# Performance work log

Hardware: AMD Instinct MI355X
Metric: run time of the kernel (lower is better)

Reference implementation:

```python
import jax, jax.numpy as jnp
import numpy as np

D_MODEL = 128
NHEAD = 8
NLAYERS = 6
LAYER_NAMES = ['self', 'cross', 'self', 'cross', 'self', 'cross']
TEMPERATURE = 5.0
EPS = 1e-6


def _pos_encoding(x):
    # Sinusoidal 1D position encoding along the width axis. x: [N, H, W, C]
    C, W = x.shape[-1], x.shape[2]
    pos = jnp.arange(W, dtype=x.dtype)[:, None]                      # [W,1]
    div = jnp.exp(jnp.arange(0, C, 2, dtype=x.dtype) * (-np.log(10000.0) / C))
    pe = jnp.zeros((W, C), x.dtype)
    pe = pe.at[:, 0::2].set(jnp.sin(pos * div))
    pe = pe.at[:, 1::2].set(jnp.cos(pos * div))
    return x + pe[None, None]                                        # broadcast over N,H


def _linear_attention(q, k, v):
    # q,k,v: [N, H, W, nhead, dim]; kernelized linear attention along W
    Q = jax.nn.elu(q) + 1.0
    K = jax.nn.elu(k) + 1.0
    v_len = v.shape[2]
    V = v / v_len
    KV = jnp.einsum('nhsed,nhsev->nhedv', K, V)                      # [N,H,e,d,d]
    Z = 1.0 / (jnp.einsum('nhled,nhed->nhle', Q, K.sum(axis=2)) + EPS)
    return jnp.einsum('nhled,nhedv,nhle->nhlev', Q, KV, Z) * v_len


def _layer_norm(x, g, b):
    m = x.mean(-1, keepdims=True)
    v = jnp.mean((x - m) ** 2, -1, keepdims=True)
    return (x - m) / jnp.sqrt(v + 1e-5) * g + b


def _encoder_layer(x, source, Wq, Wk, Wv, Wm, W1, W2, g1, b1, g2, b2):
    x = _pos_encoding(x)
    source = _pos_encoding(source)
    bs, h, w, c = x.shape
    e, d = NHEAD, c // NHEAD
    q = (x @ Wq).reshape(bs, h, w, e, d)
    k = (source @ Wk).reshape(bs, h, w, e, d)
    v = (source @ Wv).reshape(bs, h, w, e, d)
    msg = _linear_attention(q, k, v).reshape(bs, h, w, c) @ Wm
    msg = _layer_norm(msg, g1, b1)
    msg = jnp.concatenate([x, msg], axis=-1)                         # [N,H,W,2C]
    msg = jax.nn.relu(msg @ W1) @ W2
    msg = _layer_norm(msg, g2, b2)
    return x + msg


def _forward(feat0, feat1, Wq, Wk, Wv, Wm, W1, W2, g1, b1, g2, b2):
    feat0 = feat0.transpose(0, 2, 3, 1)                              # [N,H,W,C]
    feat1 = feat1.transpose(0, 2, 3, 1)
    for i, name in enumerate(LAYER_NAMES):
        p = (Wq[i], Wk[i], Wv[i], Wm[i], W1[i], W2[i], g1[i], b1[i], g2[i], b2[i])
        if name == 'self':
            feat0 = _encoder_layer(feat0, feat0, *p)
            feat1 = _encoder_layer(feat1, feat1, *p)
        else:  # cross: sequential update (feat1 sees updated feat0), as in torch source
            feat0 = _encoder_layer(feat0, feat1, *p)
            feat1 = _encoder_layer(feat1, feat0, *p)
    w = feat0.shape[2]
    attn_mask = jnp.where(jnp.triu(jnp.ones((w, w), bool), 1), -jnp.inf, 0.0)
    attn_mask = attn_mask[None, None].astype(feat0.dtype)
    scale = feat0.shape[-1] ** 0.5
    sim = jnp.einsum('ntwc,ntlc->ntwl', feat0 / scale, feat1 / scale) / TEMPERATURE
    return sim + attn_mask


def setup_inputs() -> dict:
    key = jax.random.key(0)
    ks = jax.random.split(key, 12)
    N, C, H, W = 2, D_MODEL, 64, 640
    L, D = NLAYERS, D_MODEL
    s = 1.0 / np.sqrt(D)
    s2 = 1.0 / np.sqrt(2 * D)
    return {
        'feat0': jax.random.normal(ks[0], (N, C, H, W), jnp.float32),
        'feat1': jax.random.normal(ks[1], (N, C, H, W), jnp.float32),
        'Wq': jax.random.normal(ks[2], (L, D, D), jnp.float32) * s,
        'Wk': jax.random.normal(ks[3], (L, D, D), jnp.float32) * s,
        'Wv': jax.random.normal(ks[4], (L, D, D), jnp.float32) * s,
        'Wm': jax.random.normal(ks[5], (L, D, D), jnp.float32) * s,
        'W1': jax.random.normal(ks[6], (L, 2 * D, 2 * D), jnp.float32) * s2,
        'W2': jax.random.normal(ks[7], (L, 2 * D, D), jnp.float32) * s2,
        'g1': jnp.ones((L, D), jnp.float32),
        'b1': jnp.zeros((L, D), jnp.float32),
        'g2': jnp.ones((L, D), jnp.float32),
        'b2': jnp.zeros((L, D), jnp.float32),
    }


def reference(feat0, feat1, Wq, Wk, Wv, Wm, W1, W2, g1, b1, g2, b2):
    return _forward(feat0, feat1, Wq, Wk, Wv, Wm, W1, W2, g1, b1, g2, b2)
```

## Files before the change

kernel.cpp:

```cpp
#include <hip/hip_runtime.h>
#include <cmath>
#include <math.h>

#define TOK 81920
#define WDIM 640

typedef __attribute__((ext_vector_type(8))) short short8v;
typedef __attribute__((ext_vector_type(4))) float f32x4;

__device__ __forceinline__ short f2bf(float f) {
  union { float f; unsigned u; } x; x.f = f;
  unsigned r = (x.u + 0x7fffu + ((x.u >> 16) & 1u)) >> 16;
  return (short)r;
}
__device__ __forceinline__ float bf2f(short s) {
  union { unsigned u; float f; } x; x.u = ((unsigned)(unsigned short)s) << 16;
  return x.f;
}

__global__ __launch_bounds__(256) void pe_kernel(float* __restrict__ pe) {
  int id = blockIdx.x * 256 + threadIdx.x;
  if (id >= WDIM * 128) return;
  int w = id >> 7;
  int c = id & 127;
  float i2 = (float)(c & 126);
  float freq = expf(i2 * -0.071955784156063941f);
  float ang = (float)w * freq;
  pe[id] = (c & 1) ? cosf(ang) : sinf(ang);
}

__global__ __launch_bounds__(256) void tr_kernel(const float* __restrict__ in0,
                                                 const float* __restrict__ in1,
                                                 short* __restrict__ x0,
                                                 short* __restrict__ x1) {
  __shared__ float t[32][33];
  int w0 = blockIdx.x * 32;
  int c0 = blockIdx.y * 32;
  int z = blockIdx.z;
  int feat = z >> 7;
  int nh = z & 127;
  int n = nh >> 6, h = nh & 63;
  const float* in = feat ? in1 : in0;
  short* out = feat ? x1 : x0;
  int tx = threadIdx.x & 31, ty = threadIdx.x >> 5;
  const float* ip = in + ((n * 128 + c0) * 64 + h) * 640 + w0;
#pragma unroll
  for (int i = 0; i < 32; i += 8)
    t[ty + i][tx] = ip[(ty + i) * (64 * 640) + tx];
  __syncthreads();
  short* op = out + ((size_t)(n * 64 + h) * 640 + w0) * 128 + c0;
#pragma unroll
  for (int i = 0; i < 32; i += 8)
    op[(size_t)(ty + i) * 128 + tx] = f2bf(t[tx][ty + i]);
}

__global__ __launch_bounds__(256) void wprep_kernel(
    const float* __restrict__ Wq, const float* __restrict__ Wk,
    const float* __restrict__ Wv, const float* __restrict__ Wm,
    const float* __restrict__ W1, const float* __restrict__ W2,
    short* __restrict__ BT) {
  int id = blockIdx.x * 256 + threadIdx.x;
  if (id >= 6 * 163840) return;
  int layer = id / 163840;
  int r = id % 163840;
  float v;
  if (r < 65536) {
    int seg = r >> 14;
    int rr = r & 16383;
    int n = rr >> 7, k = rr & 127;
    const float* W = seg == 0 ? Wq : seg == 1 ? Wk : seg == 2 ? Wv : Wm;
    v = W[layer * 16384 + k * 128 + n];
  } else if (r < 131072) {
    int rr = r - 65536;
    int n = rr >> 8, k = rr & 255;
    v = W1[layer * 65536 + k * 256 + n];
  } else {
    int rr = r - 131072;
    int n = rr >> 8, k = rr & 255;
    v = W2[layer * 32768 + k * 128 + n];
  }
  BT[id] = f2bf(v);
}

__device__ __forceinline__ void load_af(const short* __restrict__ A,
                                        const float* __restrict__ pe,
                                        int bm, int wr, int l15, int lk,
                                        short8v af[4][4]) {
  const int wbase = bm % WDIM;
#pragma unroll
  for (int mf = 0; mf < 4; ++mf) {
    const int rl = wr * 64 + mf * 16 + l15;
    const short* ar = A + (size_t)(bm + rl) * 128;
    const float* pr = pe + (size_t)(wbase + rl) * 128;
#pragma unroll
    for (int ks = 0; ks < 4; ++ks) {
      const int kloc = ks * 32 + lk * 8;
      short8v xa = *(const short8v*)(ar + kloc);
      f32x4 p0 = *(const f32x4*)(pr + kloc);
      f32x4 p1 = *(const f32x4*)(pr + kloc + 4);
      short8v o;
      o[0] = f2bf(bf2f(xa[0]) + p0[0]); o[1] = f2bf(bf2f(xa[1]) + p0[1]);
      o[2] = f2bf(bf2f(xa[2]) + p0[2]); o[3] = f2bf(bf2f(xa[3]) + p0[3]);
      o[4] = f2bf(bf2f(xa[4]) + p1[0]); o[5] = f2bf(bf2f(xa[5]) + p1[1]);
      o[6] = f2bf(bf2f(xa[6]) + p1[2]); o[7] = f2bf(bf2f(xa[7]) + p1[3]);
      af[ks][mf] = o;
    }
  }
}

__device__ __forceinline__ void proj_pass(const short8v af[4][4],
                                          const short* __restrict__ WT,
                                          int bm, int wr, int wc, int l15, int lk,
                                          short* __restrict__ out) {
  f32x4 acc[4][4] = {};
#pragma unroll
  for (int ks = 0; ks < 4; ++ks) {
    const int kloc = ks * 32 + lk * 8;
    short8v bfr[4];
#pragma unroll
    for (int nf = 0; nf < 4; ++nf)
      bfr[nf] = *(const short8v*)&WT[(size_t)(wc * 64 + nf * 16 + l15) * 128 + kloc];
#pragma unroll
    for (int mf = 0; mf < 4; ++mf)
#pragma unroll
      for (int nf = 0; nf < 4; ++nf)
        acc[mf][nf] = __builtin_amdgcn_mfma_f32_16x16x32_bf16(
            af[ks][mf], bfr[nf], acc[mf][nf], 0, 0, 0);
  }
#pragma unroll
  for (int mf = 0; mf < 4; ++mf)
#pragma unroll
    for (int nf = 0; nf < 4; ++nf) {
      const int colL = wc * 64 + nf * 16 + l15;
#pragma unroll
      for (int r = 0; r < 4; ++r) {
        const int row = bm + wr * 64 + mf * 16 + lk * 4 + r;
        out[(size_t)row * 128 + colL] = f2bf(acc[mf][nf][r]);
      }
    }
}

__global__ __launch_bounds__(256) void qkv_self_kernel(
    const short* __restrict__ x0, const short* __restrict__ x1,
    const float* __restrict__ pe,
    const short* __restrict__ wqT, const short* __restrict__ wkT,
    const short* __restrict__ wvT,
    short* q0, short* k0, short* v0, short* q1, short* k1, short* v1) {
  const int tid = threadIdx.x, lane = tid & 63, wid = tid >> 6;
  const int wr = wid >> 1, wc = wid & 1;
  const int bm = blockIdx.x * 128;
  const int l15 = lane & 15, lk = lane >> 4;
  const int z = blockIdx.z;
  const short* A = z ? x1 : x0;
  short8v af[4][4];
  load_af(A, pe, bm, wr, l15, lk, af);
  proj_pass(af, wqT, bm, wr, wc, l15, lk, z ? q1 : q0);
  proj_pass(af, wkT, bm, wr, wc, l15, lk, z ? k1 : k0);
  proj_pass(af, wvT, bm, wr, wc, l15, lk, z ? v1 : v0);
}

__global__ __launch_bounds__(256) void qkv_cross_kernel(
    const short* __restrict__ xq, const short* __restrict__ xs,
    const float* __restrict__ pe,
    const short* __restrict__ wqT, const short* __restrict__ wkT,
    const short* __restrict__ wvT,
    short* qb, short* kb, short* vb) {
  const int tid = threadIdx.x, lane = tid & 63, wid = tid >> 6;
  const int wr = wid >> 1, wc = wid & 1;
  const int bm = blockIdx.x * 128;
  const int l15 = lane & 15, lk = lane >> 4;
  short8v af[4][4];
  if (blockIdx.y == 0) {
    load_af(xq, pe, bm, wr, l15, lk, af);
    proj_pass(af, wqT, bm, wr, wc, l15, lk, qb);
  } else {
    load_af(xs, pe, bm, wr, l15, lk, af);
    proj_pass(af, wkT, bm, wr, wc, l15, lk, kb);
    proj_pass(af, wvT, bm, wr, wc, l15, lk, vb);
  }
}

template <int DUAL>
__global__ __launch_bounds__(256) void attn_kernel(
    const short* q0, const short* __restrict__ k0, const short* __restrict__ v0,
    const short* q1, const short* __restrict__ k1, const short* __restrict__ v1) {
  const int fid = blockIdx.x;
  const int per8 = DUAL ? 32 : 16;
  const int c8 = fid & 7, kk_ = fid >> 3;
  const int s = c8 * per8 + (kk_ >> 3);
  const int e = kk_ & 7;
  const bool f1 = DUAL && (s >= 128);
  const short* qb = f1 ? q1 : q0;
  const short* kb = f1 ? k1 : k0;
  const short* vb = f1 ? v1 : v0;
  short* ob = const_cast<short*>(qb);
  const int nh = s & 127;
  const size_t base = (size_t)nh * (640 * 128) + e * 16;

  __shared__ float Ks[128][16];
  __shared__ float Vs[128][16];
  __shared__ float KVs[16][17];
  __shared__ float Ksum[16];
  const int tid = threadIdx.x;
  const int d = tid >> 4;
  const int vv = tid & 15;
  const int srow = tid >> 1, shalf = (tid & 1) * 8;
  float kv = 0.f, ks = 0.f;
  for (int s0 = 0; s0 < 640; s0 += 128) {
    short8v k8 = *(const short8v*)&kb[base + (size_t)(s0 + srow) * 128 + shalf];
    short8v v8 = *(const short8v*)&vb[base + (size_t)(s0 + srow) * 128 + shalf];
#pragma unroll
    for (int j = 0; j < 8; ++j) {
      float kr = bf2f(k8[j]);
      Ks[srow][shalf + j] = kr > 0.f ? kr + 1.f : __expf(kr);
      Vs[srow][shalf + j] = bf2f(v8[j]);
    }
    __syncthreads();
#pragma unroll 8
    for (int sl = 0; sl < 128; ++sl) {
      float kk = Ks[sl][d];
      kv = fmaf(kk, Vs[sl][vv], kv);
      ks += kk;
    }
    __syncthreads();
  }
  KVs[d][vv] = kv;
  if (vv == 0) Ksum[d] = ks;
  __syncthreads();
  const int lane = tid & 63;
  const int wv = tid >> 6;
  const int rr = lane >> 4;
  const int cc = lane & 15;
  float kvc[16], ksr[16];
#pragma unroll
  for (int dd = 0; dd < 16; ++dd) { kvc[dd] = KVs[dd][cc]; ksr[dd] = Ksum[dd]; }
  for (int l0 = wv * 4; l0 < 640; l0 += 16) {
    int l = l0 + rr;
    float qraw = bf2f(qb[base + (size_t)l * 128 + cc]);
    float qe = qraw > 0.f ? qraw + 1.f : __expf(qraw);
    float o = 0.f, dz = 0.f;
#pragma unroll
    for (int dd = 0; dd < 16; ++dd) {
      float qv = __shfl(qe, rr * 16 + dd);
      o = fmaf(qv, kvc[dd], o);
      dz = fmaf(qv, ksr[dd], dz);
    }
    ob[base + (size_t)l * 128 + cc] = f2bf(o / (dz + 1e-6f));
  }
}

__global__ __launch_bounds__(256) void wm_w1_kernel(
    const short* __restrict__ oA, const short* __restrict__ oB,
    const short* __restrict__ xA, const short* __restrict__ xB,
    const float* __restrict__ pe, const short* __restrict__ wmT,
    const short* __restrict__ w1T, const float* __restrict__ g,
    const float* __restrict__ b,
    short* h0A, short* h1A, short* h0B, short* h1B) {
  const int z = blockIdx.z;
  const short* o = z ? oB : oA;
  const short* x = z ? xB : xA;
  short* h0 = z ? h0B : h0A;
  short* h1 = z ? h1B : h1A;
  __shared__ short msgS[128][136];
  __shared__ float lds_s[2][128];
  __shared__ float lds_q[2][128];
  const int tid = threadIdx.x, lane = tid & 63, wid = tid >> 6;
  const int wr = wid >> 1, wc = wid & 1;
  const int bm = blockIdx.x * 128;
  const int l15 = lane & 15, lk = lane >> 4;
  f32x4 acc[4][4] = {};
#pragma unroll
  for (int ks = 0; ks < 4; ++ks) {
    const int kloc = ks * 32 + lk * 8;
    short8v bfr[4], afr[4];
#pragma unroll
    for (int nf = 0; nf < 4; ++nf)
      bfr[nf] = *(const short8v*)&wmT[(size_t)(wc * 64 + nf * 16 + l15) * 128 + kloc];
#pragma unroll
    for (int mf = 0; mf < 4; ++mf)
      afr[mf] = *(const short8v*)&o[(size_t)(bm + wr * 64 + mf * 16 + l15) * 128 + kloc];
#pragma unroll
    for (int mf = 0; mf < 4; ++mf)
#pragma unroll
      for (int nf = 0; nf < 4; ++nf)
        acc[mf][nf] = __builtin_amdgcn_mfma_f32_16x16x32_bf16(
            afr[mf], bfr[nf], acc[mf][nf], 0, 0, 0);
  }
#pragma unroll
  for (int mf = 0; mf < 4; ++mf)
#pragma unroll
    for (int r = 0; r < 4; ++r) {
      float s = acc[mf][0][r] + acc[mf][1][r] + acc[mf][2][r] + acc[mf][3][r];
      float qq = acc[mf][0][r] * acc[mf][0][r] + acc[mf][1][r] * acc[mf][1][r]
               + acc[mf][2][r] * acc[mf][2][r] + acc[mf][3][r] * acc[mf][3][r];
#pragma unroll
      for (int off = 1; off < 16; off <<= 1) {
        s += __shfl_xor(s, off);
        qq += __shfl_xor(qq, off);
      }
      if (l15 == 0) {
        int rl = wr * 64 + mf * 16 + lk * 4 + r;
        lds_s[wc][rl] = s;
        lds_q[wc][rl] = qq;
      }
    }
  __syncthreads();
  float gv[4], bv[4];
#pragma unroll
  for (int nf = 0; nf < 4; ++nf) {
    int c = wc * 64 + nf * 16 + l15;
    gv[nf] = g[c]; bv[nf] = b[c];
  }
#pragma unroll
  for (int mf = 0; mf < 4; ++mf)
#pragma unroll
    for (int r = 0; r < 4; ++r) {
      int rl = wr * 64 + mf * 16 + lk * 4 + r;
      float mean = (lds_s[0][rl] + lds_s[1][rl]) * (1.f / 128.f);
      float var = (lds_q[0][rl] + lds_q[1][rl]) * (1.f / 128.f) - mean * mean;
      float rstd = rsqrtf(var + 1e-5f);
#pragma unroll
      for (int nf = 0; nf < 4; ++nf) {
        float val = (acc[mf][nf][r] - mean) * rstd * gv[nf] + bv[nf];
        msgS[rl][wc * 64 + nf * 16 + l15] = f2bf(val);
      }
    }
  __syncthreads();
#pragma unroll
  for (int p = 0; p < 2; ++p) {
    f32x4 acc2[4][4] = {};
#pragma unroll
    for (int ks = 0; ks < 8; ++ks) {
      const int kloc = ks * 32 + lk * 8;
      short8v bfr[4], afr[4];
#pragma unroll
      for (int nf = 0; nf < 4; ++nf)
        bfr[nf] = *(const short8v*)&w1T[(size_t)(p * 128 + wc * 64 + nf * 16 + l15) * 256 + kloc];
      if (ks < 4) {
        const int wbase = bm % WDIM;
#pragma unroll
        for (int mf = 0; mf < 4; ++mf) {
          const int rl = wr * 64 + mf * 16 + l15;
          short8v xa = *(const short8v*)(x + (size_t)(bm + rl) * 128 + kloc);
          const float* pr = pe + (size_t)(wbase + rl) * 128 + kloc;
          f32x4 p0 = *(const f32x4*)pr;
          f32x4 p1 = *(const f32x4*)(pr + 4);
          short8v ov;
          ov[0] = f2bf(bf2f(xa[0]) + p0[0]); ov[1] = f2bf(bf2f(xa[1]) + p0[1]);
          ov[2] = f2bf(bf2f(xa[2]) + p0[2]); ov[3] = f2bf(bf2f(xa[3]) + p0[3]);
          ov[4] = f2bf(bf2f(xa[4]) + p1[0]); ov[5] = f2bf(bf2f(xa[5]) + p1[1]);
          ov[6] = f2bf(bf2f(xa[6]) + p1[2]); ov[7] = f2bf(bf2f(xa[7]) + p1[3]);
          afr[mf] = ov;
        }
      } else {
#pragma unroll
        for (int mf = 0; mf < 4; ++mf)
          afr[mf] = *(const short8v*)&msgS[wr * 64 + mf * 16 + l15][kloc - 128];
      }
#pragma unroll
      for (int mf = 0; mf < 4; ++mf)
#pragma unroll
        for (int nf = 0; nf < 4; ++nf)
          acc2[mf][nf] = __builtin_amdgcn_mfma_f32_16x16x32_bf16(
              afr[mf], bfr[nf], acc2[mf][nf], 0, 0, 0);
    }
    short* h = p ? h1 : h0;
#pragma unroll
    for (int mf = 0; mf < 4; ++mf)
#pragma unroll
      for (int nf = 0; nf < 4; ++nf) {
        const int colL = wc * 64 + nf * 16 + l15;
#pragma unroll
        for (int r = 0; r < 4; ++r) {
          const int row = bm + wr * 64 + mf * 16 + lk * 4 + r;
          h[(size_t)row * 128 + colL] = f2bf(fmaxf(acc2[mf][nf][r], 0.f));
        }
      }
  }
}

__global__ __launch_bounds__(256) void w2_ln_kernel(
    const short* __restrict__ h0A, const short* __restrict__ h1A,
    const short* __restrict__ h0B, const short* __restrict__ h1B,
    const short* __restrict__ w2T, short* xA, short* xB,
    const float* __restrict__ pe, const float* __restrict__ g,
    const float* __restrict__ b) {
  const int z = blockIdx.z;
  const short* h0 = z ? h0B : h0A;
  const short* h1 = z ? h1B : h1A;
  short* x = z ? xB : xA;
  __shared__ float lds_s[2][128];
  __shared__ float lds_q[2][128];
  const int tid = threadIdx.x, lane = tid & 63, wid = tid >> 6;
  const int wr = wid >> 1, wc = wid & 1;
  const int bm = blockIdx.x * 128;
  const int l15 = lane & 15, lk = lane >> 4;
  const int wbase = bm % WDIM;
  f32x4 acc[4][4] = {};
#pragma unroll
  for (int ks = 0; ks < 8; ++ks) {
    const int kloc = ks * 32 + lk * 8;
    const short* hp = (ks < 4) ? h0 : h1;
    const int kl = (ks < 4) ? kloc : kloc - 128;
    short8v bfr[4], afr[4];
#pragma unroll
    for (int nf = 0; nf < 4; ++nf)
      bfr[nf] = *(const short8v*)&w2T[(size_t)(wc * 64 + nf * 16 + l15) * 256 + kloc];
#pragma unroll
    for (int mf = 0; mf < 4; ++mf)
      afr[mf] = *(const short8v*)&hp[(size_t)(bm + wr * 64 + mf * 16 + l15) * 128 + kl];
#pragma unroll
    for (int mf = 0; mf < 4; ++mf)
#pragma unroll
      for (int nf = 0; nf < 4; ++nf)
        acc[mf][nf] = __builtin_amdgcn_mfma_f32_16x16x32_bf16(
            afr[mf], bfr[nf], acc[mf][nf], 0, 0, 0);
  }
#pragma unroll
  for (int mf = 0; mf < 4; ++mf)
#pragma unroll
    for (int r = 0; r < 4; ++r) {
      float s = acc[mf][0][r] + acc[mf][1][r] + acc[mf][2][r] + acc[mf][3][r];
      float qq = acc[mf][0][r] * acc[mf][0][r] + acc[mf][1][r] * acc[mf][1][r]
               + acc[mf][2][r] * acc[mf][2][r] + acc[mf][3][r] * acc[mf][3][r];
#pragma unroll
      for (int off = 1; off < 16; off <<= 1) {
        s += __shfl_xor(s, off);
        qq += __shfl_xor(qq, off);
      }
      if (l15 == 0) {
        int rl = wr * 64 + mf * 16 + lk * 4 + r;
        lds_s[wc][rl] = s;
        lds_q[wc][rl] = qq;
      }
    }
  __syncthreads();
  float gv[4], bv[4];
#pragma unroll
  for (int nf = 0; nf < 4; ++nf) {
    int c = wc * 64 + nf * 16 + l15;
    gv[nf] = g[c]; bv[nf] = b[c];
  }
#pragma unroll
  for (int mf = 0; mf < 4; ++mf)
#pragma unroll
    for (int r = 0; r < 4; ++r) {
      int rl = wr * 64 + mf * 16 + lk * 4 + r;
      float mean = (lds_s[0][rl] + lds_s[1][rl]) * (1.f / 128.f);
      float var = (lds_q[0][rl] + lds_q[1][rl]) * (1.f / 128.f) - mean * mean;
      float rstd = rsqrtf(var + 1e-5f);
      int row = bm + rl;
#pragma unroll
      for (int nf = 0; nf < 4; ++nf) {
        int col = wc * 64 + nf * 16 + l15;
        float ln = (acc[mf][nf][r] - mean) * rstd * gv[nf] + bv[nf];
        size_t xi = (size_t)row * 128 + col;
        float xv = bf2f(x[xi]) + pe[(size_t)(wbase + rl) * 128 + col] + ln;
        x[xi] = f2bf(xv);
      }
    }
}

__global__ __launch_bounds__(256) void sim_mfma(const short* __restrict__ f0,
                                                const short* __restrict__ f1,
                                                float* __restrict__ out) {
  const int fid = (blockIdx.z * 5 + blockIdx.y) * 5 + blockIdx.x;
  const int c8 = fid & 7, kk_ = fid >> 3;
  const int nt = c8 * 16 + kk_ / 25;
  const int r2 = kk_ % 25;
  const int bw = (r2 % 5) * 128;
  const int bl = (r2 / 5) * 128;
  const int tid = threadIdx.x;
  const int lane = tid & 63;
  const int wid = tid >> 6;
  const int wr = wid >> 1, wc = wid & 1;
  const short* __restrict__ A = f0 + (size_t)nt * 640 * 128;
  const short* __restrict__ B = f1 + (size_t)nt * 640 * 128;
  const int l15 = lane & 15;
  const int lk = lane >> 4;
  f32x4 acc[4][4] = {};
#pragma unroll
  for (int ks = 0; ks < 4; ++ks) {
    const int kloc = ks * 32 + lk * 8;
    short8v afr[4], bfr[4];
#pragma unroll
    for (int mf = 0; mf < 4; ++mf)
      afr[mf] = *(const short8v*)&A[(size_t)(bw + wr * 64 + mf * 16 + l15) * 128 + kloc];
#pragma unroll
    for (int nf = 0; nf < 4; ++nf)
      bfr[nf] = *(const short8v*)&B[(size_t)(bl + wc * 64 + nf * 16 + l15) * 128 + kloc];
#pragma unroll
    for (int mf = 0; mf < 4; ++mf)
#pragma unroll
      for (int nf = 0; nf < 4; ++nf)
        acc[mf][nf] = __builtin_amdgcn_mfma_f32_16x16x32_bf16(
            afr[mf], bfr[nf], acc[mf][nf], 0, 0, 0);
  }
#pragma unroll
  for (int mf = 0; mf < 4; ++mf)
#pragma unroll
    for (int nf = 0; nf < 4; ++nf) {
      const int l = bl + wc * 64 + nf * 16 + l15;
#pragma unroll
      for (int r = 0; r < 4; ++r) {
        const int w = bw + wr * 64 + mf * 16 + lk * 4 + r;
        float v = acc[mf][nf][r] * (1.f / 640.f);
        if (l > w) v = -1e30f;
        out[((size_t)nt * 640 + w) * 640 + l] = v;
      }
    }
}

extern "C" void kernel_launch(void* const* d_in, const int* in_sizes, int n_in,
                              void* d_out, int out_size, void* d_ws, size_t ws_size,
                              hipStream_t stream) {
  (void)in_sizes; (void)n_in; (void)out_size; (void)ws_size;
  const float* feat0 = (const float*)d_in[0];
  const float* feat1 = (const float*)d_in[1];
  const float* Wq = (const float*)d_in[2];
  const float* Wk = (const float*)d_in[3];
  const float* Wv = (const float*)d_in[4];
  const float* Wm = (const float*)d_in[5];
  const float* W1 = (const float*)d_in[6];
  const float* W2 = (const float*)d_in[7];
  const float* g1 = (const float*)d_in[8];
  const float* b1 = (const float*)d_in[9];
  const float* g2 = (const float*)d_in[10];
  const float* b2 = (const float*)d_in[11];

  float* wsf = (float*)d_ws;
  const size_t U = (size_t)TOK * 128;
  float* pe = wsf;
  short* x0 = (short*)(wsf + 81920);
  short* x1 = x0 + U;
  short* q0 = x1 + U;
  short* k0 = q0 + U;
  short* v0 = k0 + U;
  short* q1 = v0 + U;
  short* k1 = q1 + U;
  short* v1 = k1 + U;
  short* bt = v1 + U;

  dim3 blk(256);
  pe_kernel<<<dim3(320), blk, 0, stream>>>(pe);
  tr_kernel<<<dim3(20, 4, 256), blk, 0, stream>>>(feat0, feat1, x0, x1);
  wprep_kernel<<<dim3((6 * 163840 + 255) / 256), blk, 0, stream>>>(
      Wq, Wk, Wv, Wm, W1, W2, bt);

  const int NB = TOK / 128;
  for (int i = 0; i < 6; ++i) {
    const short* bt_i = bt + (size_t)i * 163840;
    const short* wqT = bt_i;
    const short* wkT = bt_i + 16384;
    const short* wvT = bt_i + 32768;
    const short* wmT = bt_i + 49152;
    const short* w1T = bt_i + 65536;
    const short* w2T = bt_i + 131072;
    const float* g1_i = g1 + i * 128;
    const float* b1_i = b1 + i * 128;
    const float* g2_i = g2 + i * 128;
    const float* b2_i = b2 + i * 128;
    if ((i & 1) == 0) {
      qkv_self_kernel<<<dim3(NB, 1, 2), blk, 0, stream>>>(
          x0, x1, pe, wqT, wkT, wvT, q0, k0, v0, q1, k1, v1);
      attn_kernel<1><<<dim3(2048), blk, 0, stream>>>(q0, k0, v0, q1, k1, v1);
      wm_w1_kernel<<<dim3(NB, 1, 2), blk, 0, stream>>>(
          q0, q1, x0, x1, pe, wmT, w1T, g1_i, b1_i, k0, v0, k1, v1);
      w2_ln_kernel<<<dim3(NB, 1, 2), blk, 0, stream>>>(
          k0, v0, k1, v1, w2T, x0, x1, pe, g2_i, b2_i);
    } else {
      qkv_cross_kernel<<<dim3(NB, 2), blk, 0, stream>>>(
          x0, x1, pe, wqT, wkT, wvT, q0, k0, v0);
      attn_kernel<0><<<dim3(1024), blk, 0, stream>>>(q0, k0, v0, q0, k0, v0);
      wm_w1_kernel<<<dim3(NB, 1, 1), blk, 0, stream>>>(
          q0, q0, x0, x0, pe, wmT, w1T, g1_i, b1_i, k0, v0, k0, v0);
      w2_ln_kernel<<<dim3(NB, 1, 1), blk, 0, stream>>>(
          k0, v0, k0, v0, w2T, x0, x0, pe, g2_i, b2_i);

      qkv_cross_kernel<<<dim3(NB, 2), blk, 0, stream>>>(
          x1, x0, pe, wqT, wkT, wvT, q0, k0, v0);
      attn_kernel<0><<<dim3(1024), blk, 0, stream>>>(q0, k0, v0, q0, k0, v0);
      wm_w1_kernel<<<dim3(NB, 1, 1), blk, 0, stream>>>(
          q0, q0, x1, x1, pe, wmT, w1T, g1_i, b1_i, k0, v0, k0, v0);
      w2_ln_kernel<<<dim3(NB, 1, 1), blk, 0, stream>>>(
          k0, v0, k0, v0, w2T, x1, x1, pe, g2_i, b2_i);
    }
  }
  sim_mfma<<<dim3(5, 5, 128), blk, 0, stream>>>(x0, x1, (float*)d_out);
}
```

Baseline: 2.780 ms.

## Split wm+w1 kernel, recompute A fragments per projection, raise occupancy bounds

The QKV projection no longer keeps all A fragments in registers. It reloads and re-adds the position encoding per k-step for each projection, which lowers register pressure. The fused Wm+LayerNorm+W1 kernel is split into two kernels, with the LayerNorm output written to global memory in place of shared memory. The split frees LDS, and launch_bounds(256,4) requests higher occupancy. In exchange there are extra global loads, an extra kernel launch per layer step, and the A input is re-read three times in the QKV projection.

```diff
diff --git a/kernel.cpp b/kernel.cpp
--- a/kernel.cpp
+++ b/kernel.cpp
@@ -82,50 +82,40 @@
   BT[id] = f2bf(v);
 }
 
-__device__ __forceinline__ void load_af(const short* __restrict__ A,
-                                        const float* __restrict__ pe,
-                                        int bm, int wr, int l15, int lk,
-                                        short8v af[4][4]) {
+__device__ __forceinline__ void proj_one(const short* __restrict__ A,
+                                         const float* __restrict__ pe,
+                                         const short* __restrict__ WT,
+                                         int bm, int wr, int wc, int l15, int lk,
+                                         short* __restrict__ out) {
   const int wbase = bm % WDIM;
-#pragma unroll
-  for (int mf = 0; mf < 4; ++mf) {
-    const int rl = wr * 64 + mf * 16 + l15;
-    const short* ar = A + (size_t)(bm + rl) * 128;
-    const float* pr = pe + (size_t)(wbase + rl) * 128;
-#pragma unroll
-    for (int ks = 0; ks < 4; ++ks) {
-      const int kloc = ks * 32 + lk * 8;
-      short8v xa = *(const short8v*)(ar + kloc);
-      f32x4 p0 = *(const f32x4*)(pr + kloc);
-      f32x4 p1 = *(const f32x4*)(pr + kloc + 4);
+  f32x4 acc[4][4] = {};
+#pragma unroll
+  for (int ks = 0; ks < 4; ++ks) {
+    const int kloc = ks * 32 + lk * 8;
+    short8v bfr[4], afr[4];
+#pragma unroll
+    for (int nf = 0; nf < 4; ++nf)
+      bfr[nf] = *(const short8v*)&WT[(size_t)(wc * 64 + nf * 16 + l15) * 128 + kloc];
+#pragma unroll
+    for (int mf = 0; mf < 4; ++mf) {
+      const int rl = wr * 64 + mf * 16 + l15;
+      short8v xa = *(const short8v*)(A + (size_t)(bm + rl) * 128 + kloc);
+      const float* pr = pe + (size_t)(wbase + rl) * 128 + kloc;
+      f32x4 p0 = *(const f32x4*)pr;
+      f32x4 p1 = *(const f32x4*)(pr + 4);
       short8v o;
       o[0] = f2bf(bf2f(xa[0]) + p0[0]); o[1] = f2bf(bf2f(xa[1]) + p0[1]);
       o[2] = f2bf(bf2f(xa[2]) + p0[2]); o[3] = f2bf(bf2f(xa[3]) + p0[3]);
       o[4] = f2bf(bf2f(xa[4]) + p1[0]); o[5] = f2bf(bf2f(xa[5]) + p1[1]);
       o[6] = f2bf(bf2f(xa[6]) + p1[2]); o[7] = f2bf(bf2f(xa[7]) + p1[3]);
-      af[ks][mf] = o;
-    }
-  }
-}
-
-__device__ __forceinline__ void proj_pass(const short8v af[4][4],
-                                          const short* __restrict__ WT,
-                                          int bm, int wr, int wc, int l15, int lk,
-                                          short* __restrict__ out) {
-  f32x4 acc[4][4] = {};
-#pragma unroll
-  for (int ks = 0; ks < 4; ++ks) {
-    const int kloc = ks * 32 + lk * 8;
-    short8v bfr[4];
-#pragma unroll
-    for (int nf = 0; nf < 4; ++nf)
-      bfr[nf] = *(const short8v*)&WT[(size_t)(wc * 64 + nf * 16 + l15) * 128 + kloc];
+      afr[mf] = o;
+    }
 #pragma unroll
     for (int mf = 0; mf < 4; ++mf)
 #pragma unroll
       for (int nf = 0; nf < 4; ++nf)
         acc[mf][nf] = __builtin_amdgcn_mfma_f32_16x16x32_bf16(
-            af[ks][mf], bfr[nf], acc[mf][nf], 0, 0, 0);
+            afr[mf], bfr[nf], acc[mf][nf], 0, 0, 0);
   }
 #pragma unroll
   for (int mf = 0; mf < 4; ++mf)
@@ -140,7 +130,7 @@
     }
 }
 
-__global__ __launch_bounds__(256) void qkv_self_kernel(
+__global__ __launch_bounds__(256, 4) void qkv_self_kernel(
     const short* __restrict__ x0, const short* __restrict__ x1,
     const float* __restrict__ pe,
     const short* __restrict__ wqT, const short* __restrict__ wkT,
@@ -152,14 +142,12 @@
   const int l15 = lane & 15, lk = lane >> 4;
   const int z = blockIdx.z;
   const short* A = z ? x1 : x0;
-  short8v af[4][4];
-  load_af(A, pe, bm, wr, l15, lk, af);
-  proj_pass(af, wqT, bm, wr, wc, l15, lk, z ? q1 : q0);
-  proj_pass(af, wkT, bm, wr, wc, l15, lk, z ? k1 : k0);
-  proj_pass(af, wvT, bm, wr, wc, l15, lk, z ? v1 : v0);
-}
-
-__global__ __launch_bounds__(256) void qkv_cross_kernel(
+  proj_one(A, pe, wqT, bm, wr, wc, l15, lk, z ? q1 : q0);
+  proj_one(A, pe, wkT, bm, wr, wc, l15, lk, z ? k1 : k0);
+  proj_one(A, pe, wvT, bm, wr, wc, l15, lk, z ? v1 : v0);
+}
+
+__global__ __launch_bounds__(256, 4) void qkv_cross_kernel(
     const short* __restrict__ xq, const short* __restrict__ xs,
     const float* __restrict__ pe,
     const short* __restrict__ wqT, const short* __restrict__ wkT,
@@ -169,14 +157,11 @@
   const int wr = wid >> 1, wc = wid & 1;
   const int bm = blockIdx.x * 128;
   const int l15 = lane & 15, lk = lane >> 4;
-  short8v af[4][4];
   if (blockIdx.y == 0) {
-    load_af(xq, pe, bm, wr, l15, lk, af);
-    proj_pass(af, wqT, bm, wr, wc, l15, lk, qb);
+    proj_one(xq, pe, wqT, bm, wr, wc, l15, lk, qb);
   } else {
-    load_af(xs, pe, bm, wr, l15, lk, af);
-    proj_pass(af, wkT, bm, wr, wc, l15, lk, kb);
-    proj_pass(af, wvT, bm, wr, wc, l15, lk, vb);
+    proj_one(xs, pe, wkT, bm, wr, wc, l15, lk, kb);
+    proj_one(xs, pe, wvT, bm, wr, wc, l15, lk, vb);
   }
 }
 
@@ -249,19 +234,11 @@
   }
 }
 
-__global__ __launch_bounds__(256) void wm_w1_kernel(
-    const short* __restrict__ oA, const short* __restrict__ oB,
-    const short* __restrict__ xA, const short* __restrict__ xB,
-    const float* __restrict__ pe, const short* __restrict__ wmT,
-    const short* __restrict__ w1T, const float* __restrict__ g,
-    const float* __restrict__ b,
-    short* h0A, short* h1A, short* h0B, short* h1B) {
+__global__ __launch_bounds__(256, 4) void wm_ln_kernel(
+    short* oA, short* oB, const short* __restrict__ wmT,
+    const float* __restrict__ g, const float* __restrict__ b) {
   const int z = blockIdx.z;
-  const short* o = z ? oB : oA;
-  const short* x = z ? xB : xA;
-  short* h0 = z ? h0B : h0A;
-  short* h1 = z ? h1B : h1A;
-  __shared__ short msgS[128][136];
+  short* o = z ? oB : oA;
   __shared__ float lds_s[2][128];
   __shared__ float lds_q[2][128];
   const int tid = threadIdx.x, lane = tid & 63, wid = tid >> 6;
@@ -322,13 +299,28 @@
 #pragma unroll
       for (int nf = 0; nf < 4; ++nf) {
         float val = (acc[mf][nf][r] - mean) * rstd * gv[nf] + bv[nf];
-        msgS[rl][wc * 64 + nf * 16 + l15] = f2bf(val);
-      }
-    }
-  __syncthreads();
-#pragma unroll
+        o[(size_t)(bm + rl) * 128 + wc * 64 + nf * 16 + l15] = f2bf(val);
+      }
+    }
+}
+
+__global__ __launch_bounds__(256, 4) void w1_kernel(
+    const short* __restrict__ xA, const short* __restrict__ xB,
+    const short* __restrict__ mA, const short* __restrict__ mB,
+    const float* __restrict__ pe, const short* __restrict__ w1T,
+    short* h0A, short* h1A, short* h0B, short* h1B) {
+  const int z = blockIdx.z;
+  const short* x = z ? xB : xA;
+  const short* m = z ? mB : mA;
+  short* h0 = z ? h0B : h0A;
+  short* h1 = z ? h1B : h1A;
+  const int tid = threadIdx.x, lane = tid & 63, wid = tid >> 6;
+  const int wr = wid >> 1, wc = wid & 1;
+  const int bm = blockIdx.x * 128;
+  const int l15 = lane & 15, lk = lane >> 4;
+  const int wbase = bm % WDIM;
   for (int p = 0; p < 2; ++p) {
-    f32x4 acc2[4][4] = {};
+    f32x4 acc[4][4] = {};
 #pragma unroll
     for (int ks = 0; ks < 8; ++ks) {
       const int kloc = ks * 32 + lk * 8;
@@ -337,7 +329,6 @@
       for (int nf = 0; nf < 4; ++nf)
         bfr[nf] = *(const short8v*)&w1T[(size_t)(p * 128 + wc * 64 + nf * 16 + l15) * 256 + kloc];
       if (ks < 4) {
-        const int wbase = bm % WDIM;
 #pragma unroll
         for (int mf = 0; mf < 4; ++mf) {
           const int rl = wr * 64 + mf * 16 + l15;
@@ -355,14 +346,14 @@
       } else {
 #pragma unroll
         for (int mf = 0; mf < 4; ++mf)
-          afr[mf] = *(const short8v*)&msgS[wr * 64 + mf * 16 + l15][kloc - 128];
+          afr[mf] = *(const short8v*)&m[(size_t)(bm + wr * 64 + mf * 16 + l15) * 128 + kloc - 128];
       }
 #pragma unroll
       for (int mf = 0; mf < 4; ++mf)
 #pragma unroll
         for (int nf = 0; nf < 4; ++nf)
-          acc2[mf][nf] = __builtin_amdgcn_mfma_f32_16x16x32_bf16(
-              afr[mf], bfr[nf], acc2[mf][nf], 0, 0, 0);
+          acc[mf][nf] = __builtin_amdgcn_mfma_f32_16x16x32_bf16(
+              afr[mf], bfr[nf], acc[mf][nf], 0, 0, 0);
     }
     short* h = p ? h1 : h0;
 #pragma unroll
@@ -373,13 +364,13 @@
 #pragma unroll
         for (int r = 0; r < 4; ++r) {
           const int row = bm + wr * 64 + mf * 16 + lk * 4 + r;
-          h[(size_t)row * 128 + colL] = f2bf(fmaxf(acc2[mf][nf][r], 0.f));
+          h[(size_t)row * 128 + colL] = f2bf(fmaxf(acc[mf][nf][r], 0.f));
         }
       }
   }
 }
 
-__global__ __launch_bounds__(256) void w2_ln_kernel(
+__global__ __launch_bounds__(256, 4) void w2_ln_kernel(
     const short* __restrict__ h0A, const short* __restrict__ h1A,
     const short* __restrict__ h0B, const short* __restrict__ h1B,
     const short* __restrict__ w2T, short* xA, short* xB,
@@ -564,24 +555,27 @@
       qkv_self_kernel<<<dim3(NB, 1, 2), blk, 0, stream>>>(
           x0, x1, pe, wqT, wkT, wvT, q0, k0, v0, q1, k1, v1);
       attn_kernel<1><<<dim3(2048), blk, 0, stream>>>(q0, k0, v0, q1, k1, v1);
-      wm_w1_kernel<<<dim3(NB, 1, 2), blk, 0, stream>>>(
-          q0, q1, x0, x1, pe, wmT, w1T, g1_i, b1_i, k0, v0, k1, v1);
+      wm_ln_kernel<<<dim3(NB, 1, 2), blk, 0, stream>>>(q0, q1, wmT, g1_i, b1_i);
+      w1_kernel<<<dim3(NB, 1, 2), blk, 0, stream>>>(
+          x0, x1, q0, q1, pe, w1T, k0, v0, k1, v1);
       w2_ln_kernel<<<dim3(NB, 1, 2), blk, 0, stream>>>(
           k0, v0, k1, v1, w2T, x0, x1, pe, g2_i, b2_i);
     } else {
       qkv_cross_kernel<<<dim3(NB, 2), blk, 0, stream>>>(
           x0, x1, pe, wqT, wkT, wvT, q0, k0, v0);
       attn_kernel<0><<<dim3(1024), blk, 0, stream>>>(q0, k0, v0, q0, k0, v0);
-      wm_w1_kernel<<<dim3(NB, 1, 1), blk, 0, stream>>>(
-          q0, q0, x0, x0, pe, wmT, w1T, g1_i, b1_i, k0, v0, k0, v0);
+      wm_ln_kernel<<<dim3(NB, 1, 1), blk, 0, stream>>>(q0, q0, wmT, g1_i, b1_i);
+      w1_kernel<<<dim3(NB, 1, 1), blk, 0, stream>>>(
+          x0, x0, q0, q0, pe, w1T, k0, v0, k0, v0);
       w2_ln_kernel<<<dim3(NB, 1, 1), blk, 0, stream>>>(
           k0, v0, k0, v0, w2T, x0, x0, pe, g2_i, b2_i);
 
       qkv_cross_kernel<<<dim3(NB, 2), blk, 0, stream>>>(
           x1, x0, pe, wqT, wkT, wvT, q0, k0, v0);
       attn_kernel<0><<<dim3(1024), blk, 0, stream>>>(q0, k0, v0, q0, k0, v0);
-      wm_w1_kernel<<<dim3(NB, 1, 1), blk, 0, stream>>>(
-          q0, q0, x1, x1, pe, wmT, w1T, g1_i, b1_i, k0, v0, k0, v0);
+      wm_ln_kernel<<<dim3(NB, 1, 1), blk, 0, stream>>>(q0, q0, wmT, g1_i, b1_i);
+      w1_kernel<<<dim3(NB, 1, 1), blk, 0, stream>>>(
+          x1, x1, q0, q0, pe, w1T, k0, v0, k0, v0);
       w2_ln_kernel<<<dim3(NB, 1, 1), blk, 0, stream>>>(
           k0, v0, k0, v0, w2T, x1, x1, pe, g2_i, b2_i);
     }
```

Measured after the change: 4.245 ms. 52.7% more time.
